# Optimization experiments

Hardware: AMD Instinct MI355X
Metric: run time of the kernel (lower is better)

## Reference

```python
import jax, jax.numpy as jnp
import numpy as np

EMBED = 1024
HEADS = 16
HEAD_DIM = EMBED // HEADS
B, T = 2, 2048
ROPE_THETA = 10000.0


def _rope(x):
    # x: [B, H, T, D]; standard half-split rotary embedding, applied per head
    D = x.shape[-1]
    inv_freq = 1.0 / (ROPE_THETA ** (jnp.arange(0, D, 2, dtype=jnp.float32) / D))  # [D/2]
    freqs = jnp.arange(x.shape[2], dtype=jnp.float32)[:, None] * inv_freq[None, :]  # [T, D/2]
    cos = jnp.cos(freqs).astype(x.dtype)  # [T, D/2]
    sin = jnp.sin(freqs).astype(x.dtype)
    x1, x2 = x[..., : D // 2], x[..., D // 2 :]
    return jnp.concatenate([x1 * cos - x2 * sin, x2 * cos + x1 * sin], axis=-1)


def setup_inputs() -> dict:
    key = jax.random.key(0)
    ks = jax.random.split(key, 5)
    s = 1.0 / np.sqrt(EMBED)
    return {
        "x": jax.random.normal(ks[0], (B, T, EMBED), dtype=jnp.float32),
        "Wq": jax.random.normal(ks[1], (EMBED, EMBED), dtype=jnp.float32) * s,
        "bq": jnp.zeros((EMBED,), dtype=jnp.float32),
        "Wk": jax.random.normal(ks[2], (EMBED, EMBED), dtype=jnp.float32) * s,
        "bk": jnp.zeros((EMBED,), dtype=jnp.float32),
        "Wv": jax.random.normal(ks[3], (EMBED, EMBED), dtype=jnp.float32) * s,
        "bv": jnp.zeros((EMBED,), dtype=jnp.float32),
        "Wo": jax.random.normal(ks[4], (EMBED, EMBED), dtype=jnp.float32) * s,
        "bo": jnp.zeros((EMBED,), dtype=jnp.float32),
    }


def reference(x, Wq, bq, Wk, bk, Wv, bv, Wo, bo):
    Bb, Tt, C = x.shape
    H, D = HEADS, HEAD_DIM
    # torch Linear: y = x @ W.T + b
    def proj(W, b):
        return (jnp.einsum("btc,oc->bto", x, W) + b).reshape(Bb, Tt, H, D).transpose(0, 2, 1, 3)

    q = _rope(proj(Wq, bq))  # [B, H, T, D]
    k = _rope(proj(Wk, bk))
    v = proj(Wv, bv)
    scale = jnp.sqrt(jnp.asarray(D, dtype=x.dtype))
    scores = jnp.einsum("bhtd,bhsd->bhts", q, k) / scale  # [B, H, T, T]
    attn = jax.nn.softmax(scores, axis=-1)  # dropout = identity in eval mode
    out = jnp.einsum("bhts,bhsd->bhtd", attn, v)  # [B, H, T, D]
    out = out.transpose(0, 2, 1, 3).reshape(Bb, Tt, C)
    return jnp.einsum("btc,oc->bto", out, Wo) + bo
```

## Files before the change

kernel.cpp:

```cpp
#include <hip/hip_runtime.h>
#include <hip/hip_bf16.h>

#define EMBED 1024
#define HEADS 16
#define HDIM 64
#define BATCH 2
#define SEQ 2048
#define MTOT (BATCH*SEQ)

typedef __attribute__((ext_vector_type(2))) float f32x2;
typedef __attribute__((ext_vector_type(4))) float f32x4;
typedef __attribute__((ext_vector_type(16))) float f32x16;
typedef __attribute__((ext_vector_type(4))) short s16x4;
typedef __attribute__((ext_vector_type(8))) short bf16x8;
typedef __attribute__((ext_vector_type(4))) int i32x4;

static __device__ __forceinline__ short f2bf(float f) {
  unsigned u = __builtin_bit_cast(unsigned, f);
  unsigned r = (u + 0x7fffu + ((u >> 16) & 1u)) >> 16;
  return (short)r;
}
static __device__ __forceinline__ float bf2f(short s) {
  unsigned u = ((unsigned)(unsigned short)s) << 16;
  return __builtin_bit_cast(float, u);
}
static __device__ __forceinline__ int pack2bf_fast(float lo, float hi) {
  unsigned ulo = __builtin_bit_cast(unsigned, lo) + 0x8000u;
  unsigned uhi = __builtin_bit_cast(unsigned, hi) + 0x8000u;
  int r;
  asm("v_cvt_pk_bf16_f32 %0, %1, %2" : "=v"(r)
      : "v"(__builtin_bit_cast(float, ulo)), "v"(__builtin_bit_cast(float, uhi)));
  return r;
}
static __device__ __forceinline__ void pswap(int &a, int &b) {
  asm("v_permlane32_swap_b32 %0, %1" : "+v"(a), "+v"(b));
}

typedef __attribute__((address_space(1))) const void gvoid_t;
typedef __attribute__((address_space(3))) void lvoid_t;
static __device__ __forceinline__ void gload_lds16(const void* g, void* l) {
  __builtin_amdgcn_global_load_lds((gvoid_t*)g, (lvoid_t*)l, 16, 0, 0);
}

__global__ __launch_bounds__(256) void cvt_bf16(
    const float* __restrict__ x,
    const float* __restrict__ Wq, const float* __restrict__ Wk,
    const float* __restrict__ Wv, const float* __restrict__ Wo,
    short* __restrict__ xb,
    short* __restrict__ Wqb, short* __restrict__ Wkb,
    short* __restrict__ Wvb, short* __restrict__ Wob,
    f32x2* __restrict__ tab)
{
  int i = blockIdx.x * 256 + threadIdx.x;
  if (i >= 2097152) {
    int i2 = i - 2097152;
    int t = i2 >> 5, j = i2 & 31;
    float invf = exp2f(-(float)j * 0.4152410118609203f);
    float sn, cs;
    sincosf((float)t * invf, &sn, &cs);
    f32x2 e; e[0] = cs; e[1] = sn;
    tab[i2] = e;
    return;
  }
  const float* src; short* dst; int off;
  if (i < 1048576) { src = x; dst = xb; off = i; }
  else {
    int j = i - 1048576;
    int w = j >> 18; off = j & 262143;
    src = (w == 0) ? Wq : (w == 1) ? Wk : (w == 2) ? Wv : Wo;
    dst = (w == 0) ? Wqb : (w == 1) ? Wkb : (w == 2) ? Wvb : Wob;
  }
  f32x4 v = ((const f32x4*)src)[off];
  s16x4 h;
#pragma unroll
  for (int j = 0; j < 4; ++j) h[j] = f2bf(v[j]);
  ((s16x4*)dst)[off] = h;
}

__global__ __launch_bounds__(256) void qkv_gemm(
    const short* __restrict__ xb,
    const short* __restrict__ Wqb, const short* __restrict__ Wkb, const short* __restrict__ Wvb,
    const float* __restrict__ bq, const float* __restrict__ bk, const float* __restrict__ bv,
    const f32x2* __restrict__ tab,
    short* __restrict__ Qb, short* __restrict__ Kb, short* __restrict__ Vb)
{
  __shared__ short As[128][64];
  __shared__ short Bs[128][64];
  int tid = threadIdx.x;
  int lane = tid & 63, wid = tid >> 6;
  int wm = wid >> 1, wn = wid & 1;
  int bm = blockIdx.x / 24;
  int bncol = blockIdx.x % 24;
  int wsel = bncol >> 3, bnn = bncol & 7;
  const short* W    = (wsel == 0) ? Wqb : (wsel == 1) ? Wkb : Wvb;
  const float* bias = (wsel == 0) ? bq : (wsel == 1) ? bk : bv;

  f32x4 acc[4][4] = {};

  const short* Abase = xb + (size_t)bm * 128 * EMBED;
  const short* Bbase = W + (size_t)bnn * 128 * EMBED;
  char* AsB = (char*)&As[0][0];
  char* BsB = (char*)&Bs[0][0];

  for (int kt = 0; kt < EMBED / 64; ++kt) {
#pragma unroll
    for (int i = 0; i < 4; ++i) {
      int s = tid + i * 256;
      int row = s >> 3, c = s & 7;
      int cs = c ^ (row & 7);
      gload_lds16(&Abase[(size_t)row * EMBED + kt * 64 + cs * 8],
                  AsB + i * 4096 + wid * 1024 + lane * 16);
      gload_lds16(&Bbase[(size_t)row * EMBED + kt * 64 + cs * 8],
                  BsB + i * 4096 + wid * 1024 + lane * 16);
    }
    __syncthreads();
#pragma unroll
    for (int kk = 0; kk < 2; ++kk) {
      int cp = ((kk * 4 + (lane >> 4)) ^ (lane & 7)) * 8;
      bf16x8 af[4], bfr[4];
#pragma unroll
      for (int mf = 0; mf < 4; ++mf)
        af[mf] = *(const bf16x8*)&As[wm * 64 + mf * 16 + (lane & 15)][cp];
#pragma unroll
      for (int nf = 0; nf < 4; ++nf)
        bfr[nf] = *(const bf16x8*)&Bs[wn * 64 + nf * 16 + (lane & 15)][cp];
      if (wsel == 2) {
#pragma unroll
        for (int mf = 0; mf < 4; ++mf)
#pragma unroll
          for (int nf = 0; nf < 4; ++nf)
            acc[mf][nf] = __builtin_amdgcn_mfma_f32_16x16x32_bf16(bfr[mf], af[nf], acc[mf][nf], 0, 0, 0);
      } else {
#pragma unroll
        for (int mf = 0; mf < 4; ++mf)
#pragma unroll
          for (int nf = 0; nf < 4; ++nf)
            acc[mf][nf] = __builtin_amdgcn_mfma_f32_16x16x32_bf16(af[mf], bfr[nf], acc[mf][nf], 0, 0, 0);
      }
    }
    __syncthreads();
  }

  if (wsel < 2) {
    short* dst = (wsel == 0) ? Qb : Kb;
    float sc = (wsel == 0) ? 0.18033688011112042f : 1.0f;
#pragma unroll
    for (int nf = 0; nf < 2; ++nf) {
      int col = bnn * 128 + wn * 64 + nf * 16 + (lane & 15);
      int h = col >> 6, j = col & 31;
      float b1 = bias[col], b2 = bias[col + 32];
#pragma unroll
      for (int mf = 0; mf < 4; ++mf) {
        int row0 = bm * 128 + wm * 64 + mf * 16 + ((lane >> 4) << 2);
#pragma unroll
        for (int r = 0; r < 4; ++r) {
          int m = row0 + r;
          int b_ = m >> 11, t = m & (SEQ - 1);
          f32x2 e = tab[t * 32 + j];
          float a1 = acc[mf][nf][r] + b1;
          float a2 = acc[mf][nf + 2][r] + b2;
          size_t o = (((size_t)(b_ * HEADS + h)) * SEQ + t) * HDIM + j;
          dst[o]      = f2bf((a1 * e[0] - a2 * e[1]) * sc);
          dst[o + 32] = f2bf((a2 * e[0] + a1 * e[1]) * sc);
        }
      }
    }
  } else {
#pragma unroll
    for (int mf = 0; mf < 4; ++mf) {
#pragma unroll
      for (int r = 0; r < 4; ++r) {
        int cch = bnn * 128 + wn * 64 + mf * 16 + ((lane >> 4) << 2) + r;
        int h = cch >> 6, d = cch & 63;
        float bb = bias[cch];
#pragma unroll
        for (int nf = 0; nf < 4; ++nf) {
          int m = bm * 128 + wm * 64 + nf * 16 + (lane & 15);
          int b_ = m >> 11, t = m & (SEQ - 1);
          Vb[((size_t)(b_ * HEADS + h) * HDIM + d) * SEQ + t] = f2bf(acc[mf][nf][r] + bb);
        }
      }
    }
  }
}

#define QBLK 128
#define KBLK 64

__global__ __launch_bounds__(256, 2) void attn_kernel(
    const short* __restrict__ Qb, const short* __restrict__ Kb,
    const short* __restrict__ Vb, short* __restrict__ Ob)
{
  __shared__ short Ks[2][KBLK][68];
  __shared__ short Vs[2][HDIM][68];

  int tid = threadIdx.x, lane = tid & 63, wid = tid >> 6;
  int l31 = lane & 31, lhi = lane >> 5;

  int bid = blockIdx.x;
  int swz = (bid & 7) * 64 + (bid >> 3);
  int qi = swz & 15, bh = swz >> 4;
  int b = bh >> 4, h = bh & 15;

  const short* Qp = Qb + ((size_t)bh * SEQ + qi * QBLK + wid * 32) * HDIM;
  const short* Kp = Kb + (size_t)bh * SEQ * HDIM;
  const short* Vp = Vb + (size_t)bh * HDIM * SEQ;

  bf16x8 qf[4];
#pragma unroll
  for (int cc = 0; cc < 4; ++cc)
    qf[cc] = *(const bf16x8*)&Qp[(size_t)l31 * HDIM + cc * 16 + lhi * 8];

  f32x16 oacc0 = {}, oacc1 = {}, lacc = {};
  bf16x8 vones;
#pragma unroll
  for (int j = 0; j < 8; ++j) vones[j] = (short)0x3F80;

  bf16x8 kreg[2], vreg[2];
#pragma unroll
  for (int i = 0; i < 2; ++i) {
    int s = tid + i * 256;
    kreg[i] = *(const bf16x8*)&Kp[(size_t)(s >> 3) * HDIM + (s & 7) * 8];
    vreg[i] = *(const bf16x8*)&Vp[(size_t)(s >> 3) * SEQ + (s & 7) * 8];
  }
#pragma unroll
  for (int i = 0; i < 2; ++i) {
    int s = tid + i * 256;
    *(bf16x8*)&Ks[0][s >> 3][(s & 7) * 8] = kreg[i];
    *(bf16x8*)&Vs[0][s >> 3][(s & 7) * 8] = vreg[i];
  }
  __syncthreads();

  for (int kt = 0; kt < SEQ / KBLK; ++kt) {
    int cur = kt & 1;
    if (kt + 1 < SEQ / KBLK) {
#pragma unroll
      for (int i = 0; i < 2; ++i) {
        int s = tid + i * 256;
        kreg[i] = *(const bf16x8*)&Kp[(size_t)((kt + 1) * KBLK + (s >> 3)) * HDIM + (s & 7) * 8];
        vreg[i] = *(const bf16x8*)&Vp[(size_t)(s >> 3) * SEQ + (kt + 1) * KBLK + (s & 7) * 8];
      }
    }

    f32x16 s0 = {}, s1 = {};
#pragma unroll
    for (int cc = 0; cc < 4; ++cc) {
      bf16x8 a0 = *(const bf16x8*)&Ks[cur][l31][cc * 16 + lhi * 8];
      bf16x8 a1 = *(const bf16x8*)&Ks[cur][32 + l31][cc * 16 + lhi * 8];
      s0 = __builtin_amdgcn_mfma_f32_32x32x16_bf16(a0, qf[cc], s0, 0, 0, 0);
      s1 = __builtin_amdgcn_mfma_f32_32x32x16_bf16(a1, qf[cc], s1, 0, 0, 0);
    }
    f32x16 p0, p1;
#pragma unroll
    for (int i = 0; i < 16; ++i) {
      p0[i] = __builtin_amdgcn_exp2f(s0[i]);
      p1[i] = __builtin_amdgcn_exp2f(s1[i]);
    }

#pragma unroll
    for (int c = 0; c < 2; ++c) {
      int w0 = pack2bf_fast(p0[8 * c + 0], p0[8 * c + 1]);
      int w1 = pack2bf_fast(p0[8 * c + 2], p0[8 * c + 3]);
      int w2 = pack2bf_fast(p0[8 * c + 4], p0[8 * c + 5]);
      int w3 = pack2bf_fast(p0[8 * c + 6], p0[8 * c + 7]);
      pswap(w0, w2);
      pswap(w1, w3);
      i32x4 pw; pw[0] = w0; pw[1] = w1; pw[2] = w2; pw[3] = w3;
      bf16x8 pa = __builtin_bit_cast(bf16x8, pw);

      bf16x8 vf0 = *(const bf16x8*)&Vs[cur][l31][c * 16 + lhi * 8];
      bf16x8 vf1 = *(const bf16x8*)&Vs[cur][32 + l31][c * 16 + lhi * 8];
      lacc = __builtin_amdgcn_mfma_f32_32x32x16_bf16(pa, vones, lacc, 0, 0, 0);
      oacc0 = __builtin_amdgcn_mfma_f32_32x32x16_bf16(pa, vf0, oacc0, 0, 0, 0);
      oacc1 = __builtin_amdgcn_mfma_f32_32x32x16_bf16(pa, vf1, oacc1, 0, 0, 0);
    }
#pragma unroll
    for (int c = 0; c < 2; ++c) {
      int w0 = pack2bf_fast(p1[8 * c + 0], p1[8 * c + 1]);
      int w1 = pack2bf_fast(p1[8 * c + 2], p1[8 * c + 3]);
      int w2 = pack2bf_fast(p1[8 * c + 4], p1[8 * c + 5]);
      int w3 = pack2bf_fast(p1[8 * c + 6], p1[8 * c + 7]);
      pswap(w0, w2);
      pswap(w1, w3);
      i32x4 pw; pw[0] = w0; pw[1] = w1; pw[2] = w2; pw[3] = w3;
      bf16x8 pa = __builtin_bit_cast(bf16x8, pw);

      bf16x8 vf0 = *(const bf16x8*)&Vs[cur][l31][32 + c * 16 + lhi * 8];
      bf16x8 vf1 = *(const bf16x8*)&Vs[cur][32 + l31][32 + c * 16 + lhi * 8];
      lacc = __builtin_amdgcn_mfma_f32_32x32x16_bf16(pa, vones, lacc, 0, 0, 0);
      oacc0 = __builtin_amdgcn_mfma_f32_32x32x16_bf16(pa, vf0, oacc0, 0, 0, 0);
      oacc1 = __builtin_amdgcn_mfma_f32_32x32x16_bf16(pa, vf1, oacc1, 0, 0, 0);
    }

    if (kt + 1 < SEQ / KBLK) {
#pragma unroll
      for (int i = 0; i < 2; ++i) {
        int s = tid + i * 256;
        *(bf16x8*)&Ks[cur ^ 1][s >> 3][(s & 7) * 8] = kreg[i];
        *(bf16x8*)&Vs[cur ^ 1][s >> 3][(s & 7) * 8] = vreg[i];
      }
      __syncthreads();
    }
  }

#pragma unroll
  for (int r = 0; r < 16; ++r) {
    int qrow = (r & 3) + 8 * (r >> 2) + 4 * lhi;
    int t = qi * QBLK + wid * 32 + qrow;
    float inv = 1.0f / lacc[r];
    size_t base = ((size_t)(b * SEQ + t)) * EMBED + h * HDIM;
    Ob[base + l31]      = f2bf(oacc0[r] * inv);
    Ob[base + 32 + l31] = f2bf(oacc1[r] * inv);
  }
}

__global__ __launch_bounds__(256) void out_gemm(
    const short* __restrict__ A, const short* __restrict__ Wob,
    const float* __restrict__ bo, float* __restrict__ C)
{
  __shared__ short As[64][64];
  __shared__ short Bs[128][64];
  int tid = threadIdx.x;
  int lane = tid & 63, wid = tid >> 6;
  int bm = blockIdx.x >> 3, bn = blockIdx.x & 7;

  f32x4 acc[8] = {};
  const short* Abase = A + (size_t)bm * 64 * EMBED;
  const short* Bbase = Wob + (size_t)bn * 128 * EMBED;
  char* AsB = (char*)&As[0][0];
  char* BsB = (char*)&Bs[0][0];

  for (int kt = 0; kt < EMBED / 64; ++kt) {
#pragma unroll
    for (int i = 0; i < 2; ++i) {
      int s = tid + i * 256;
      int row = s >> 3, c = s & 7;
      int cs = c ^ (row & 7);
      gload_lds16(&Abase[(size_t)row * EMBED + kt * 64 + cs * 8],
                  AsB + i * 4096 + wid * 1024 + lane * 16);
    }
#pragma unroll
    for (int i = 0; i < 4; ++i) {
      int s = tid + i * 256;
      int row = s >> 3, c = s & 7;
      int cs = c ^ (row & 7);
      gload_lds16(&Bbase[(size_t)row * EMBED + kt * 64 + cs * 8],
                  BsB + i * 4096 + wid * 1024 + lane * 16);
    }
    __syncthreads();
#pragma unroll
    for (int kk = 0; kk < 2; ++kk) {
      int cp = ((kk * 4 + (lane >> 4)) ^ (lane & 7)) * 8;
      bf16x8 af = *(const bf16x8*)&As[wid * 16 + (lane & 15)][cp];
#pragma unroll
      for (int nf = 0; nf < 8; ++nf) {
        bf16x8 bfr = *(const bf16x8*)&Bs[nf * 16 + (lane & 15)][cp];
        acc[nf] = __builtin_amdgcn_mfma_f32_16x16x32_bf16(af, bfr, acc[nf], 0, 0, 0);
      }
    }
    __syncthreads();
  }

#pragma unroll
  for (int nf = 0; nf < 8; ++nf) {
    int col = bn * 128 + nf * 16 + (lane & 15);
    float bb = bo[col];
    int row0 = bm * 64 + wid * 16 + ((lane >> 4) << 2);
#pragma unroll
    for (int r = 0; r < 4; ++r)
      C[(size_t)(row0 + r) * EMBED + col] = acc[nf][r] + bb;
  }
}

extern "C" void kernel_launch(void* const* d_in, const int* in_sizes, int n_in,
                              void* d_out, int out_size, void* d_ws, size_t ws_size,
                              hipStream_t stream) {
  const float* x  = (const float*)d_in[0];
  const float* Wq = (const float*)d_in[1];
  const float* bq = (const float*)d_in[2];
  const float* Wk = (const float*)d_in[3];
  const float* bk = (const float*)d_in[4];
  const float* Wv = (const float*)d_in[5];
  const float* bv = (const float*)d_in[6];
  const float* Wo = (const float*)d_in[7];
  const float* bo = (const float*)d_in[8];
  float* out = (float*)d_out;
  char* ws = (char*)d_ws;

  const size_t MB = 1u << 20;
  short* Qb  = (short*)(ws);
  short* Kb  = (short*)(ws + 8 * MB);
  short* Vb  = (short*)(ws + 16 * MB);
  short* XOb = (short*)(ws + 24 * MB);
  short* Wqb = (short*)(ws + 32 * MB);
  short* Wkb = (short*)(ws + 34 * MB);
  short* Wvb = (short*)(ws + 36 * MB);
  short* Wob = (short*)(ws + 38 * MB);
  f32x2* tab = (f32x2*)(ws + 40 * MB);

  cvt_bf16<<<dim3(8448), dim3(256), 0, stream>>>(x, Wq, Wk, Wv, Wo, XOb, Wqb, Wkb, Wvb, Wob, tab);
  qkv_gemm<<<dim3(32 * 24), dim3(256), 0, stream>>>(XOb, Wqb, Wkb, Wvb, bq, bk, bv, tab, Qb, Kb, Vb);
  attn_kernel<<<dim3(BATCH * HEADS * (SEQ / QBLK)), dim3(256), 0, stream>>>(Qb, Kb, Vb, XOb);
  out_gemm<<<dim3(64 * 8), dim3(256), 0, stream>>>(XOb, Wob, bo, out);
}
```

Before: 118.8 us.

## Double-buffer LDS tiles in QKV and output projection GEMMs

Both GEMM kernels now keep two LDS buffers for the A and B tiles. The first K tile is loaded before the loop, and each iteration issues the async global-to-LDS loads for the next tile before running the MFMAs on the current one. This lets global memory latency overlap with matrix math instead of stalling at a barrier every iteration. In exchange, LDS use per block doubles, which may lower occupancy, and the end-of-iteration barrier now also waits on the prefetch loads.

```diff
diff --git a/kernel.cpp b/kernel.cpp
--- a/kernel.cpp
+++ b/kernel.cpp
@@ -84,8 +84,8 @@
     const f32x2* __restrict__ tab,
     short* __restrict__ Qb, short* __restrict__ Kb, short* __restrict__ Vb)
 {
-  __shared__ short As[128][64];
-  __shared__ short Bs[128][64];
+  __shared__ short As[2][128][64];
+  __shared__ short Bs[2][128][64];
   int tid = threadIdx.x;
   int lane = tid & 63, wid = tid >> 6;
   int wm = wid >> 1, wn = wid & 1;
@@ -99,31 +99,47 @@
 
   const short* Abase = xb + (size_t)bm * 128 * EMBED;
   const short* Bbase = W + (size_t)bnn * 128 * EMBED;
-  char* AsB = (char*)&As[0][0];
-  char* BsB = (char*)&Bs[0][0];
+  char* AsB = (char*)&As[0][0][0];
+  char* BsB = (char*)&Bs[0][0][0];
+  const int TSZ = 128 * 64 * 2;
+
+#pragma unroll
+  for (int i = 0; i < 4; ++i) {
+    int s = tid + i * 256;
+    int row = s >> 3, c = s & 7;
+    int cs = c ^ (row & 7);
+    gload_lds16(&Abase[(size_t)row * EMBED + cs * 8],
+                AsB + i * 4096 + wid * 1024 + lane * 16);
+    gload_lds16(&Bbase[(size_t)row * EMBED + cs * 8],
+                BsB + i * 4096 + wid * 1024 + lane * 16);
+  }
+  __syncthreads();
 
   for (int kt = 0; kt < EMBED / 64; ++kt) {
-#pragma unroll
-    for (int i = 0; i < 4; ++i) {
-      int s = tid + i * 256;
-      int row = s >> 3, c = s & 7;
-      int cs = c ^ (row & 7);
-      gload_lds16(&Abase[(size_t)row * EMBED + kt * 64 + cs * 8],
-                  AsB + i * 4096 + wid * 1024 + lane * 16);
-      gload_lds16(&Bbase[(size_t)row * EMBED + kt * 64 + cs * 8],
-                  BsB + i * 4096 + wid * 1024 + lane * 16);
-    }
-    __syncthreads();
+    int cur = kt & 1;
+    if (kt + 1 < EMBED / 64) {
+#pragma unroll
+      for (int i = 0; i < 4; ++i) {
+        int s = tid + i * 256;
+        int row = s >> 3, c = s & 7;
+        int cs = c ^ (row & 7);
+        gload_lds16(&Abase[(size_t)row * EMBED + (kt + 1) * 64 + cs * 8],
+                    AsB + (cur ^ 1) * TSZ + i * 4096 + wid * 1024 + lane * 16);
+        gload_lds16(&Bbase[(size_t)row * EMBED + (kt + 1) * 64 + cs * 8],
+                    BsB + (cur ^ 1) * TSZ + i * 4096 + wid * 1024 + lane * 16);
+      }
+    }
+
 #pragma unroll
     for (int kk = 0; kk < 2; ++kk) {
       int cp = ((kk * 4 + (lane >> 4)) ^ (lane & 7)) * 8;
       bf16x8 af[4], bfr[4];
 #pragma unroll
       for (int mf = 0; mf < 4; ++mf)
-        af[mf] = *(const bf16x8*)&As[wm * 64 + mf * 16 + (lane & 15)][cp];
+        af[mf] = *(const bf16x8*)&As[cur][wm * 64 + mf * 16 + (lane & 15)][cp];
 #pragma unroll
       for (int nf = 0; nf < 4; ++nf)
-        bfr[nf] = *(const bf16x8*)&Bs[wn * 64 + nf * 16 + (lane & 15)][cp];
+        bfr[nf] = *(const bf16x8*)&Bs[cur][wn * 64 + nf * 16 + (lane & 15)][cp];
       if (wsel == 2) {
 #pragma unroll
         for (int mf = 0; mf < 4; ++mf)
@@ -318,8 +334,8 @@
     const short* __restrict__ A, const short* __restrict__ Wob,
     const float* __restrict__ bo, float* __restrict__ C)
 {
-  __shared__ short As[64][64];
-  __shared__ short Bs[128][64];
+  __shared__ short As[2][64][64];
+  __shared__ short Bs[2][128][64];
   int tid = threadIdx.x;
   int lane = tid & 63, wid = tid >> 6;
   int bm = blockIdx.x >> 3, bn = blockIdx.x & 7;
@@ -327,34 +343,57 @@
   f32x4 acc[8] = {};
   const short* Abase = A + (size_t)bm * 64 * EMBED;
   const short* Bbase = Wob + (size_t)bn * 128 * EMBED;
-  char* AsB = (char*)&As[0][0];
-  char* BsB = (char*)&Bs[0][0];
+  char* AsB = (char*)&As[0][0][0];
+  char* BsB = (char*)&Bs[0][0][0];
+  const int ATSZ = 64 * 64 * 2;
+  const int BTSZ = 128 * 64 * 2;
+
+#pragma unroll
+  for (int i = 0; i < 2; ++i) {
+    int s = tid + i * 256;
+    int row = s >> 3, c = s & 7;
+    int cs = c ^ (row & 7);
+    gload_lds16(&Abase[(size_t)row * EMBED + cs * 8],
+                AsB + i * 4096 + wid * 1024 + lane * 16);
+  }
+#pragma unroll
+  for (int i = 0; i < 4; ++i) {
+    int s = tid + i * 256;
+    int row = s >> 3, c = s & 7;
+    int cs = c ^ (row & 7);
+    gload_lds16(&Bbase[(size_t)row * EMBED + cs * 8],
+                BsB + i * 4096 + wid * 1024 + lane * 16);
+  }
+  __syncthreads();
 
   for (int kt = 0; kt < EMBED / 64; ++kt) {
-#pragma unroll
-    for (int i = 0; i < 2; ++i) {
-      int s = tid + i * 256;
-      int row = s >> 3, c = s & 7;
-      int cs = c ^ (row & 7);
-      gload_lds16(&Abase[(size_t)row * EMBED + kt * 64 + cs * 8],
-                  AsB + i * 4096 + wid * 1024 + lane * 16);
-    }
-#pragma unroll
-    for (int i = 0; i < 4; ++i) {
-      int s = tid + i * 256;
-      int row = s >> 3, c = s & 7;
-      int cs = c ^ (row & 7);
-      gload_lds16(&Bbase[(size_t)row * EMBED + kt * 64 + cs * 8],
-                  BsB + i * 4096 + wid * 1024 + lane * 16);
-    }
-    __syncthreads();
+    int cur = kt & 1;
+    if (kt + 1 < EMBED / 64) {
+#pragma unroll
+      for (int i = 0; i < 2; ++i) {
+        int s = tid + i * 256;
+        int row = s >> 3, c = s & 7;
+        int cs = c ^ (row & 7);
+        gload_lds16(&Abase[(size_t)row * EMBED + (kt + 1) * 64 + cs * 8],
+                    AsB + (cur ^ 1) * ATSZ + i * 4096 + wid * 1024 + lane * 16);
+      }
+#pragma unroll
+      for (int i = 0; i < 4; ++i) {
+        int s = tid + i * 256;
+        int row = s >> 3, c = s & 7;
+        int cs = c ^ (row & 7);
+        gload_lds16(&Bbase[(size_t)row * EMBED + (kt + 1) * 64 + cs * 8],
+                    BsB + (cur ^ 1) * BTSZ + i * 4096 + wid * 1024 + lane * 16);
+      }
+    }
+
 #pragma unroll
     for (int kk = 0; kk < 2; ++kk) {
       int cp = ((kk * 4 + (lane >> 4)) ^ (lane & 7)) * 8;
-      bf16x8 af = *(const bf16x8*)&As[wid * 16 + (lane & 15)][cp];
+      bf16x8 af = *(const bf16x8*)&As[cur][wid * 16 + (lane & 15)][cp];
 #pragma unroll
       for (int nf = 0; nf < 8; ++nf) {
-        bf16x8 bfr = *(const bf16x8*)&Bs[nf * 16 + (lane & 15)][cp];
+        bf16x8 bfr = *(const bf16x8*)&Bs[cur][nf * 16 + (lane & 15)][cp];
         acc[nf] = __builtin_amdgcn_mfma_f32_16x16x32_bf16(af, bfr, acc[nf], 0, 0, 0);
       }
     }
```

Result: no change. 117.8 us (-0.8%).
